# Kernel tuning notes

Measured on AMD Instinct MI355X. Metric: run time of the kernel, lower is better.

The kernel has to match this reference:

```python
import jax, jax.numpy as jnp
import numpy as np

IN_DIM, HID, OUT_DIM, BATCH, T = 512, 1024, 512, 4096, 32

def setup_inputs() -> dict:
    key = jax.random.key(0)
    ks = jax.random.split(key, 7)
    s_in = 1.0 / np.sqrt(IN_DIM)
    s_h = 1.0 / np.sqrt(HID)
    return {
        "x": jax.random.normal(ks[0], (IN_DIM, BATCH), dtype=jnp.float32),
        "W_in": jax.random.normal(ks[1], (HID, IN_DIM), dtype=jnp.float32) * s_in,
        "b_in": jax.random.normal(ks[2], (HID, 1), dtype=jnp.float32) * 0.01,
        "W_rec": jax.random.normal(ks[3], (HID, HID), dtype=jnp.float32) * s_h,
        "b_rec": jax.random.normal(ks[4], (HID, 1), dtype=jnp.float32) * 0.01,
        "W_out": jax.random.normal(ks[5], (OUT_DIM, HID), dtype=jnp.float32) * s_h,
        "b_out": jax.random.normal(ks[6], (OUT_DIM, 1), dtype=jnp.float32) * 0.01,
    }

def reference(x, W_in, b_in, W_rec, b_rec, W_out, b_out):
    # initial projection: [H, B]
    y0 = jax.nn.relu(W_in @ x + b_in)

    def step(h, _):
        h_next = jax.nn.relu(W_rec @ h + b_rec)
        return h_next, h_next

    h_last, hs = jax.lax.scan(step, y0, None, length=T)  # hs: [T, H, B]
    out = jax.nn.relu(W_out @ h_last + b_out)  # [O, B]
    intermediate = jnp.concatenate([y0[None], hs], axis=0)  # [T+1, H, B]
    return out, intermediate
```

## Files before the change

kernel.cpp:

```cpp
#include <hip/hip_runtime.h>
#include <hip/hip_bf16.h>

#define IN_DIM  512
#define HID     1024
#define OUT_DIM 512
#define BATCH   4096
#define T_STEPS 32

typedef __attribute__((ext_vector_type(8))) short bf16x8;
typedef __attribute__((ext_vector_type(4))) float f32x4;

__device__ inline void gload16(const void* g, void* l) {
  __builtin_amdgcn_global_load_lds(
      (const __attribute__((address_space(1))) void*)g,
      (__attribute__((address_space(3))) void*)l, 16, 0, 0);
}

__global__ __launch_bounds__(256, 2) void gemm_bt_bias_relu(
    const __hip_bfloat16* __restrict__ A,
    const __hip_bfloat16* __restrict__ B,
    const float* __restrict__ bias,
    float* __restrict__ Cf,
    __hip_bfloat16* __restrict__ Cb,
    int K, int Nld, int nx)
{
  const int nwg = gridDim.x;
  const int q   = nwg >> 3;
  const int bid = blockIdx.x;
  const int swz = (bid & 7) * q + (bid >> 3);
  const int bxi = swz % nx;
  const int byi = swz / nx;
  const int brow = byi * 128;
  const int bcol = bxi * 64;

  const int tid  = threadIdx.x;
  const int lane = tid & 63;
  const int wid  = tid >> 6;
  const int wr   = wid >> 1, wc = wid & 1;
  const int l15  = lane & 15, l4 = lane >> 4;
  const int srow = lane >> 3;
  const int schunk = (lane & 7) ^ (srow & 7);

  __shared__ __hip_bfloat16 Alds[2][128 * 64];
  __shared__ __hip_bfloat16 Blds[2][64 * 64];

  f32x4 acc[4][2] = {};
  const int nt = K >> 6;

  auto stage = [&](int ti, int buf) {
    const int kt = ti << 6;
#pragma unroll
    for (int it = 0; it < 4; ++it) {
      const int rowbase = it * 32 + wid * 8;
      gload16(A + (size_t)(brow + rowbase + srow) * K + kt + schunk * 8,
              &Alds[buf][rowbase * 64]);
    }
#pragma unroll
    for (int it = 0; it < 2; ++it) {
      const int rowbase = it * 32 + wid * 8;
      gload16(B + (size_t)(bcol + rowbase + srow) * K + kt + schunk * 8,
              &Blds[buf][rowbase * 64]);
    }
  };

  stage(0, 0);
  stage(1, 1);

  const int rxor = l15 & 7;

  for (int ti = 0; ti < nt; ++ti) {
    const int buf = ti & 1;
    if (ti < nt - 1) {
      asm volatile("s_waitcnt vmcnt(6)" ::: "memory");
    } else {
      asm volatile("s_waitcnt vmcnt(0)" ::: "memory");
    }
    __builtin_amdgcn_s_barrier();
    __builtin_amdgcn_sched_barrier(0);

    __builtin_amdgcn_s_setprio(1);
#pragma unroll
    for (int ks = 0; ks < 2; ++ks) {
      bf16x8 af[4], bfr[2];
      const int cp = ((ks * 4 + l4) ^ rxor) * 8;
#pragma unroll
      for (int m = 0; m < 4; ++m)
        af[m] = *(const bf16x8*)&Alds[buf][(wr * 64 + m * 16 + l15) * 64 + cp];
#pragma unroll
      for (int n = 0; n < 2; ++n)
        bfr[n] = *(const bf16x8*)&Blds[buf][(wc * 32 + n * 16 + l15) * 64 + cp];
#pragma unroll
      for (int m = 0; m < 4; ++m)
#pragma unroll
        for (int n = 0; n < 2; ++n)
          acc[m][n] = __builtin_amdgcn_mfma_f32_16x16x32_bf16(af[m], bfr[n], acc[m][n], 0, 0, 0);
    }
    __builtin_amdgcn_s_setprio(0);

    asm volatile("s_waitcnt lgkmcnt(0)" ::: "memory");
    __builtin_amdgcn_sched_barrier(0);
    __builtin_amdgcn_s_barrier();
    __builtin_amdgcn_sched_barrier(0);
    if (ti < nt - 2) stage(ti + 2, buf);
  }

#pragma unroll
  for (int n = 0; n < 2; ++n) {
    const int i = bcol + wc * 32 + n * 16 + l15;
    const float bv = bias[i];
#pragma unroll
    for (int m = 0; m < 4; ++m) {
      const int b0 = brow + wr * 64 + m * 16 + l4 * 4;
      f32x4 v = acc[m][n];
      f32x4 o;
      o[0] = fmaxf(v[0] + bv, 0.0f);
      o[1] = fmaxf(v[1] + bv, 0.0f);
      o[2] = fmaxf(v[2] + bv, 0.0f);
      o[3] = fmaxf(v[3] + bv, 0.0f);
      __builtin_nontemporal_store(o, (f32x4*)(Cf + (size_t)i * BATCH + b0));
      if (Cb) {
        Cb[(size_t)(b0 + 0) * Nld + i] = __float2bfloat16(o[0]);
        Cb[(size_t)(b0 + 1) * Nld + i] = __float2bfloat16(o[1]);
        Cb[(size_t)(b0 + 2) * Nld + i] = __float2bfloat16(o[2]);
        Cb[(size_t)(b0 + 3) * Nld + i] = __float2bfloat16(o[3]);
      }
    }
  }
}

__global__ __launch_bounds__(256) void f32_to_bf16(
    const float* __restrict__ in, __hip_bfloat16* __restrict__ out, int n4)
{
  int i = blockIdx.x * blockDim.x + threadIdx.x;
  if (i < n4) {
    float4 v = ((const float4*)in)[i];
    union { __hip_bfloat16 h[4]; ushort4 u; } p;
    p.h[0] = __float2bfloat16(v.x);
    p.h[1] = __float2bfloat16(v.y);
    p.h[2] = __float2bfloat16(v.z);
    p.h[3] = __float2bfloat16(v.w);
    ((ushort4*)out)[i] = p.u;
  }
}

__global__ __launch_bounds__(256) void transpose_f32_bf16(
    const float* __restrict__ in, __hip_bfloat16* __restrict__ out, int R, int C)
{
  __shared__ float tile[32][33];
  const int c0 = blockIdx.x * 32, r0 = blockIdx.y * 32;
  const int tx = threadIdx.x & 31, ty = threadIdx.x >> 5;
#pragma unroll
  for (int dy = 0; dy < 32; dy += 8)
    tile[ty + dy][tx] = in[(size_t)(r0 + ty + dy) * C + c0 + tx];
  __syncthreads();
#pragma unroll
  for (int dy = 0; dy < 32; dy += 8)
    out[(size_t)(c0 + ty + dy) * R + r0 + tx] = __float2bfloat16(tile[tx][ty + dy]);
}

extern "C" void kernel_launch(void* const* d_in, const int* in_sizes, int n_in,
                              void* d_out, int out_size, void* d_ws, size_t ws_size,
                              hipStream_t stream)
{
  const float* x     = (const float*)d_in[0];
  const float* W_in  = (const float*)d_in[1];
  const float* b_in  = (const float*)d_in[2];
  const float* W_rec = (const float*)d_in[3];
  const float* b_rec = (const float*)d_in[4];
  const float* W_out = (const float*)d_in[5];
  const float* b_out = (const float*)d_in[6];

  float* out0 = (float*)d_out;
  float* itm  = out0 + (size_t)OUT_DIM * BATCH;

  __hip_bfloat16* xT = (__hip_bfloat16*)d_ws;
  __hip_bfloat16* Wi = xT + (size_t)BATCH * IN_DIM;
  __hip_bfloat16* Wr = Wi + (size_t)HID * IN_DIM;
  __hip_bfloat16* Wo = Wr + (size_t)HID * HID;
  __hip_bfloat16* h0 = Wo + (size_t)OUT_DIM * HID;
  __hip_bfloat16* h1 = h0 + (size_t)BATCH * HID;

  transpose_f32_bf16<<<dim3(BATCH / 32, IN_DIM / 32), 256, 0, stream>>>(x, xT, IN_DIM, BATCH);
  {
    int n4 = HID * IN_DIM / 4;
    f32_to_bf16<<<(n4 + 255) / 256, 256, 0, stream>>>(W_in, Wi, n4);
  }
  {
    int n4 = HID * HID / 4;
    f32_to_bf16<<<(n4 + 255) / 256, 256, 0, stream>>>(W_rec, Wr, n4);
  }
  {
    int n4 = OUT_DIM * HID / 4;
    f32_to_bf16<<<(n4 + 255) / 256, 256, 0, stream>>>(W_out, Wo, n4);
  }

  gemm_bt_bias_relu<<<(HID / 64) * (BATCH / 128), 256, 0, stream>>>(
      xT, Wi, b_in, itm, h0, IN_DIM, HID, HID / 64);

  __hip_bfloat16* cur = h0;
  __hip_bfloat16* nxt = h1;
  for (int t = 0; t < T_STEPS; ++t) {
    float* dst = itm + (size_t)(t + 1) * HID * BATCH;
    gemm_bt_bias_relu<<<(HID / 64) * (BATCH / 128), 256, 0, stream>>>(
        cur, Wr, b_rec, dst, nxt, HID, HID, HID / 64);
    __hip_bfloat16* tmp = cur; cur = nxt; nxt = tmp;
  }

  gemm_bt_bias_relu<<<(OUT_DIM / 64) * (BATCH / 128), 256, 0, stream>>>(
      cur, Wo, b_out, out0, (__hip_bfloat16*)nullptr, HID, 0, OUT_DIM / 64);
}
```

Measured before the change: 588.3 us.

## Load A fragments directly from global into registers, bypassing LDS

The A operand (activations) is no longer staged through LDS. Each wave now owns 32 rows and loads its A fragments straight from global memory into registers with inline-asm dwordx4 loads, double-buffered in registers one k-tile ahead. Only the B (weight) tile still goes through LDS, and the wave layout changes from a 2x2 split to a 4x1 split over rows. This cuts LDS traffic and shared-memory footprint, but the A loads are uncoalesced per-row accesses, the waitcnt accounting relies on hand-written instruction counts, and register pressure rises.

Result: slower. 750.8 us (+27.6%).

```diff
diff --git a/kernel.cpp b/kernel.cpp
--- a/kernel.cpp
+++ b/kernel.cpp
@@ -14,6 +14,14 @@
   __builtin_amdgcn_global_load_lds(
       (const __attribute__((address_space(1))) void*)g,
       (__attribute__((address_space(3))) void*)l, 16, 0, 0);
+}
+
+__device__ inline void aload2(bf16x8 &d0, bf16x8 &d1, const __hip_bfloat16* p) {
+  asm volatile("global_load_dwordx4 %0, %2, off\n\t"
+               "global_load_dwordx4 %1, %2, off offset:64"
+               : "=&v"(d0), "=&v"(d1)
+               : "v"(p)
+               : "memory");
 }
 
 __global__ __launch_bounds__(256, 2) void gemm_bt_bias_relu(
@@ -36,25 +44,17 @@
   const int tid  = threadIdx.x;
   const int lane = tid & 63;
   const int wid  = tid >> 6;
-  const int wr   = wid >> 1, wc = wid & 1;
   const int l15  = lane & 15, l4 = lane >> 4;
   const int srow = lane >> 3;
   const int schunk = (lane & 7) ^ (srow & 7);
 
-  __shared__ __hip_bfloat16 Alds[2][128 * 64];
   __shared__ __hip_bfloat16 Blds[2][64 * 64];
 
-  f32x4 acc[4][2] = {};
+  f32x4 acc[2][4] = {};
   const int nt = K >> 6;
 
-  auto stage = [&](int ti, int buf) {
+  auto stageB = [&](int ti, int buf) {
     const int kt = ti << 6;
-#pragma unroll
-    for (int it = 0; it < 4; ++it) {
-      const int rowbase = it * 32 + wid * 8;
-      gload16(A + (size_t)(brow + rowbase + srow) * K + kt + schunk * 8,
-              &Alds[buf][rowbase * 64]);
-    }
 #pragma unroll
     for (int it = 0; it < 2; ++it) {
       const int rowbase = it * 32 + wid * 8;
@@ -63,37 +63,55 @@
     }
   };
 
-  stage(0, 0);
-  stage(1, 1);
-
-  const int rxor = l15 & 7;
-
-  for (int ti = 0; ti < nt; ++ti) {
+  const __hip_bfloat16* abase0 = A + (size_t)(brow + wid * 32 + l15) * K + l4 * 8;
+  const __hip_bfloat16* abase1 = abase0 + (size_t)16 * K;
+
+  bf16x8 xa00, xa01, xa10, xa11;
+  bf16x8 ya00, ya01, ya10, ya11;
+
+  stageB(0, 0);
+  __builtin_amdgcn_sched_barrier(0);
+  aload2(xa00, xa01, abase0);
+  aload2(xa10, xa11, abase1);
+  __builtin_amdgcn_sched_barrier(0);
+  stageB(1, 1);
+
+  const int rx7 = l15 & 7;
+
+  auto iter = [&](int ti,
+                  const bf16x8 &ca00, const bf16x8 &ca01,
+                  const bf16x8 &ca10, const bf16x8 &ca11,
+                  bf16x8 &na00, bf16x8 &na01, bf16x8 &na10, bf16x8 &na11) {
     const int buf = ti & 1;
     if (ti < nt - 1) {
-      asm volatile("s_waitcnt vmcnt(6)" ::: "memory");
+      asm volatile("s_waitcnt vmcnt(2)" ::: "memory");
     } else {
       asm volatile("s_waitcnt vmcnt(0)" ::: "memory");
     }
     __builtin_amdgcn_s_barrier();
     __builtin_amdgcn_sched_barrier(0);
 
+    if (ti + 1 < nt) {
+      const int koff = (ti + 1) << 6;
+      aload2(na00, na01, abase0 + koff);
+      aload2(na10, na11, abase1 + koff);
+    }
+
     __builtin_amdgcn_s_setprio(1);
 #pragma unroll
     for (int ks = 0; ks < 2; ++ks) {
-      bf16x8 af[4], bfr[2];
-      const int cp = ((ks * 4 + l4) ^ rxor) * 8;
-#pragma unroll
-      for (int m = 0; m < 4; ++m)
-        af[m] = *(const bf16x8*)&Alds[buf][(wr * 64 + m * 16 + l15) * 64 + cp];
-#pragma unroll
-      for (int n = 0; n < 2; ++n)
-        bfr[n] = *(const bf16x8*)&Blds[buf][(wc * 32 + n * 16 + l15) * 64 + cp];
-#pragma unroll
-      for (int m = 0; m < 4; ++m)
-#pragma unroll
-        for (int n = 0; n < 2; ++n)
-          acc[m][n] = __builtin_amdgcn_mfma_f32_16x16x32_bf16(af[m], bfr[n], acc[m][n], 0, 0, 0);
+      bf16x8 bfr[4];
+      const int cp = ((ks * 4 + l4) ^ rx7) * 8;
+#pragma unroll
+      for (int n = 0; n < 4; ++n)
+        bfr[n] = *(const bf16x8*)&Blds[buf][(n * 16 + l15) * 64 + cp];
+      const bf16x8 &af0 = ks ? ca01 : ca00;
+      const bf16x8 &af1 = ks ? ca11 : ca10;
+#pragma unroll
+      for (int n = 0; n < 4; ++n) {
+        acc[0][n] = __builtin_amdgcn_mfma_f32_16x16x32_bf16(af0, bfr[n], acc[0][n], 0, 0, 0);
+        acc[1][n] = __builtin_amdgcn_mfma_f32_16x16x32_bf16(af1, bfr[n], acc[1][n], 0, 0, 0);
+      }
     }
     __builtin_amdgcn_s_setprio(0);
 
@@ -101,16 +119,21 @@
     __builtin_amdgcn_sched_barrier(0);
     __builtin_amdgcn_s_barrier();
     __builtin_amdgcn_sched_barrier(0);
-    if (ti < nt - 2) stage(ti + 2, buf);
-  }
-
-#pragma unroll
-  for (int n = 0; n < 2; ++n) {
-    const int i = bcol + wc * 32 + n * 16 + l15;
+    if (ti + 2 < nt) stageB(ti + 2, buf);
+  };
+
+  for (int ti = 0; ti < nt; ti += 2) {
+    iter(ti,     xa00, xa01, xa10, xa11,  ya00, ya01, ya10, ya11);
+    iter(ti + 1, ya00, ya01, ya10, ya11,  xa00, xa01, xa10, xa11);
+  }
+
+#pragma unroll
+  for (int n = 0; n < 4; ++n) {
+    const int i = bcol + n * 16 + l15;
     const float bv = bias[i];
 #pragma unroll
-    for (int m = 0; m < 4; ++m) {
-      const int b0 = brow + wr * 64 + m * 16 + l4 * 4;
+    for (int m = 0; m < 2; ++m) {
+      const int b0 = brow + wid * 32 + m * 16 + l4 * 4;
       f32x4 v = acc[m][n];
       f32x4 o;
       o[0] = fmaxf(v[0] + bv, 0.0f);
```

## Pre-tile weights into MFMA fragment layout and load B directly to registers

Applied to the files above, without the earlier changes.

Weights are converted once into a tiled layout that matches the MFMA B-operand fragment, so each wave reads its B fragments straight from global memory into registers with dwordx4 loads. This drops the B tiles from LDS, halving LDS traffic and shared-memory footprint, and the B loads are double-buffered in registers alongside the A LDS pipeline. The three weight-conversion launches are merged into one kernel. The change adds register pressure and leaves the weight reads uncoalesced across waves, though they are L2-resident.

Measured after the change: 503.6 us. -14.4%, faster.

```diff
diff --git a/kernel.cpp b/kernel.cpp
--- a/kernel.cpp
+++ b/kernel.cpp
@@ -16,9 +16,14 @@
       (__attribute__((address_space(3))) void*)l, 16, 0, 0);
 }
 
+__device__ inline void bload(bf16x8 &d, const __hip_bfloat16* p) {
+  asm volatile("global_load_dwordx4 %0, %1, off"
+               : "=&v"(d) : "v"(p) : "memory");
+}
+
 __global__ __launch_bounds__(256, 2) void gemm_bt_bias_relu(
     const __hip_bfloat16* __restrict__ A,
-    const __hip_bfloat16* __restrict__ B,
+    const __hip_bfloat16* __restrict__ Wt,
     const float* __restrict__ bias,
     float* __restrict__ Cf,
     __hip_bfloat16* __restrict__ Cb,
@@ -42,12 +47,11 @@
   const int schunk = (lane & 7) ^ (srow & 7);
 
   __shared__ __hip_bfloat16 Alds[2][128 * 64];
-  __shared__ __hip_bfloat16 Blds[2][64 * 64];
 
   f32x4 acc[4][2] = {};
   const int nt = K >> 6;
 
-  auto stage = [&](int ti, int buf) {
+  auto stageA = [&](int ti, int buf) {
     const int kt = ti << 6;
 #pragma unroll
     for (int it = 0; it < 4; ++it) {
@@ -55,23 +59,37 @@
       gload16(A + (size_t)(brow + rowbase + srow) * K + kt + schunk * 8,
               &Alds[buf][rowbase * 64]);
     }
-#pragma unroll
-    for (int it = 0; it < 2; ++it) {
-      const int rowbase = it * 32 + wid * 8;
-      gload16(B + (size_t)(bcol + rowbase + srow) * K + kt + schunk * 8,
-              &Blds[buf][rowbase * 64]);
-    }
   };
 
-  stage(0, 0);
-  stage(1, 1);
+  const int Ks = K >> 5;
+  const __hip_bfloat16* wt[2];
+  wt[0] = Wt + (size_t)((bcol >> 4) + wc * 2 + 0) * Ks * 512 + lane * 8;
+  wt[1] = Wt + (size_t)((bcol >> 4) + wc * 2 + 1) * Ks * 512 + lane * 8;
+
+  bf16x8 bx[2][2], by[2][2];
+
+#pragma unroll
+  for (int n = 0; n < 2; ++n) {
+    bload(bx[n][0], wt[n] + 0 * 512);
+    bload(bx[n][1], wt[n] + 1 * 512);
+  }
+  __builtin_amdgcn_sched_barrier(0);
+  stageA(0, 0);
+  __builtin_amdgcn_sched_barrier(0);
+#pragma unroll
+  for (int n = 0; n < 2; ++n) {
+    bload(by[n][0], wt[n] + 2 * 512);
+    bload(by[n][1], wt[n] + 3 * 512);
+  }
+  __builtin_amdgcn_sched_barrier(0);
+  stageA(1, 1);
 
   const int rxor = l15 & 7;
 
-  for (int ti = 0; ti < nt; ++ti) {
+  auto iterf = [&](int ti, bf16x8 (&cb)[2][2]) {
     const int buf = ti & 1;
     if (ti < nt - 1) {
-      asm volatile("s_waitcnt vmcnt(6)" ::: "memory");
+      asm volatile("s_waitcnt vmcnt(8)" ::: "memory");
     } else {
       asm volatile("s_waitcnt vmcnt(0)" ::: "memory");
     }
@@ -81,27 +99,39 @@
     __builtin_amdgcn_s_setprio(1);
 #pragma unroll
     for (int ks = 0; ks < 2; ++ks) {
-      bf16x8 af[4], bfr[2];
+      bf16x8 af[4];
       const int cp = ((ks * 4 + l4) ^ rxor) * 8;
 #pragma unroll
       for (int m = 0; m < 4; ++m)
         af[m] = *(const bf16x8*)&Alds[buf][(wr * 64 + m * 16 + l15) * 64 + cp];
 #pragma unroll
-      for (int n = 0; n < 2; ++n)
-        bfr[n] = *(const bf16x8*)&Blds[buf][(wc * 32 + n * 16 + l15) * 64 + cp];
-#pragma unroll
       for (int m = 0; m < 4; ++m)
 #pragma unroll
         for (int n = 0; n < 2; ++n)
-          acc[m][n] = __builtin_amdgcn_mfma_f32_16x16x32_bf16(af[m], bfr[n], acc[m][n], 0, 0, 0);
+          acc[m][n] = __builtin_amdgcn_mfma_f32_16x16x32_bf16(af[m], cb[n][ks], acc[m][n], 0, 0, 0);
     }
     __builtin_amdgcn_s_setprio(0);
+    __builtin_amdgcn_sched_barrier(0);
+
+    if (ti + 2 < nt) {
+      const int s0 = (ti + 2) * 2;
+#pragma unroll
+      for (int n = 0; n < 2; ++n) {
+        bload(cb[n][0], wt[n] + (s0 + 0) * 512);
+        bload(cb[n][1], wt[n] + (s0 + 1) * 512);
+      }
+    }
 
     asm volatile("s_waitcnt lgkmcnt(0)" ::: "memory");
     __builtin_amdgcn_sched_barrier(0);
     __builtin_amdgcn_s_barrier();
     __builtin_amdgcn_sched_barrier(0);
-    if (ti < nt - 2) stage(ti + 2, buf);
+    if (ti + 2 < nt) stageA(ti + 2, buf);
+  };
+
+  for (int ti = 0; ti < nt; ti += 2) {
+    iterf(ti,     bx);
+    iterf(ti + 1, by);
   }
 
 #pragma unroll
@@ -128,19 +158,34 @@
   }
 }
 
-__global__ __launch_bounds__(256) void f32_to_bf16(
-    const float* __restrict__ in, __hip_bfloat16* __restrict__ out, int n4)
-{
-  int i = blockIdx.x * blockDim.x + threadIdx.x;
-  if (i < n4) {
-    float4 v = ((const float4*)in)[i];
-    union { __hip_bfloat16 h[4]; ushort4 u; } p;
-    p.h[0] = __float2bfloat16(v.x);
-    p.h[1] = __float2bfloat16(v.y);
-    p.h[2] = __float2bfloat16(v.z);
-    p.h[3] = __float2bfloat16(v.w);
-    ((ushort4*)out)[i] = p.u;
-  }
+__global__ __launch_bounds__(256) void convert_weights_tiled(
+    const float* __restrict__ w_in, const float* __restrict__ w_rec,
+    const float* __restrict__ w_out,
+    __hip_bfloat16* __restrict__ wi, __hip_bfloat16* __restrict__ wr,
+    __hip_bfloat16* __restrict__ wo)
+{
+  const int c  = blockIdx.x * blockDim.x + threadIdx.x;
+  const int c1 = HID * IN_DIM / 8;
+  const int c2 = c1 + HID * HID / 8;
+  const int c3 = c2 + OUT_DIM * HID / 8;
+  const float* src; __hip_bfloat16* dst; int K, local;
+  if (c < c1)      { src = w_in;  dst = wi; K = IN_DIM; local = c; }
+  else if (c < c2) { src = w_rec; dst = wr; K = HID;    local = c - c1; }
+  else if (c < c3) { src = w_out; dst = wo; K = HID;    local = c - c2; }
+  else return;
+  const int kc8 = K >> 3;
+  const int i  = local / kc8;
+  const int k0 = (local - i * kc8) << 3;
+  const float4 a = *(const float4*)(src + (size_t)i * K + k0);
+  const float4 b = *(const float4*)(src + (size_t)i * K + k0 + 4);
+  union { __hip_bfloat16 h[8]; bf16x8 v; } p;
+  p.h[0] = __float2bfloat16(a.x); p.h[1] = __float2bfloat16(a.y);
+  p.h[2] = __float2bfloat16(a.z); p.h[3] = __float2bfloat16(a.w);
+  p.h[4] = __float2bfloat16(b.x); p.h[5] = __float2bfloat16(b.y);
+  p.h[6] = __float2bfloat16(b.z); p.h[7] = __float2bfloat16(b.w);
+  const size_t off = ((size_t)(i >> 4) * (K >> 5) + (k0 >> 5)) * 512
+                   + ((k0 >> 3) & 3) * 128 + (i & 15) * 8;
+  *(bf16x8*)(dst + off) = p.v;
 }
 
 __global__ __launch_bounds__(256) void transpose_f32_bf16(
@@ -182,16 +227,9 @@
 
   transpose_f32_bf16<<<dim3(BATCH / 32, IN_DIM / 32), 256, 0, stream>>>(x, xT, IN_DIM, BATCH);
   {
-    int n4 = HID * IN_DIM / 4;
-    f32_to_bf16<<<(n4 + 255) / 256, 256, 0, stream>>>(W_in, Wi, n4);
-  }
-  {
-    int n4 = HID * HID / 4;
-    f32_to_bf16<<<(n4 + 255) / 256, 256, 0, stream>>>(W_rec, Wr, n4);
-  }
-  {
-    int n4 = OUT_DIM * HID / 4;
-    f32_to_bf16<<<(n4 + 255) / 256, 256, 0, stream>>>(W_out, Wo, n4);
+    const int nC = (HID * IN_DIM + HID * HID + OUT_DIM * HID) / 8;
+    convert_weights_tiled<<<(nC + 255) / 256, 256, 0, stream>>>(
+        W_in, W_rec, W_out, Wi, Wr, Wo);
   }
 
   gemm_bt_bias_relu<<<(HID / 64) * (BATCH / 128), 256, 0, stream>>>(
```
